# Kernel tuning notes

Hardware: AMD Instinct MI355X
Metric: run time of the kernel (lower is better)

Reference implementation:

```python
import jax, jax.numpy as jnp
import numpy as np

DT_SCALER = 1.0 / 24.0
ODE_STEPS = 4  # fixed-step RK4 stand-in for adaptive odeint(rtol=atol=1e-3)
B, T, D, H = 1024, 100, 32, 256
ODE_MID = 50  # hidden width of the ODE func MLP (hard-coded 50 in source)


def setup_inputs() -> dict:
    key = jax.random.key(0)
    ks = jax.random.split(key, 20)
    n = lambda k, s: jax.random.normal(k, s, dtype=jnp.float32)
    std = 0.1  # module inits weights N(0, 0.1), biases 0
    return {
        "dt": jax.random.uniform(ks[0], (B, T, 2), dtype=jnp.float32),
        "x": n(ks[1], (B, T, D)),
        # RNNCell params
        "W_ih": n(ks[2], (H, D)) * std,
        "b_ih": jnp.zeros((H,), jnp.float32),
        "W_hh": n(ks[3], (H, H)) * std,
        "b_hh": jnp.zeros((H,), jnp.float32),
        # ODE func: Linear(H,50) -> tanh -> Linear(50,H)
        "ode_w1": n(ks[4], (ODE_MID, H)) * std,
        "ode_b1": jnp.zeros((ODE_MID,), jnp.float32),
        "ode_w2": n(ks[5], (H, ODE_MID)) * std,
        "ode_b2": jnp.zeros((H,), jnp.float32),
        # mu head: l1 (H -> H//2), distribution_mu (H//2 -> 1)
        "l1_w": n(ks[6], (H // 2, H)) * std,
        "l1_b": jnp.zeros((H // 2,), jnp.float32),
        "mu_w": n(ks[7], (1, H // 2)) * std,
        "mu_b": jnp.zeros((1,), jnp.float32),
        # sigma head: Linear(H,H) -> tanh -> Linear(H,1) -> softplus
        "sig_w1": n(ks[8], (H, H)) * std,
        "sig_b1": jnp.zeros((H,), jnp.float32),
        "sig_w2": n(ks[9], (1, H)) * std,
        "sig_b2": jnp.zeros((1,), jnp.float32),
    }


def reference(dt, x, W_ih, b_ih, W_hh, b_hh, ode_w1, ode_b1, ode_w2, ode_b2,
              l1_w, l1_b, mu_w, mu_b, sig_w1, sig_b1, sig_w2, sig_b2):
    Bsz = x.shape[0]
    xs = jnp.swapaxes(x, 0, 1)                               # [T,B,D]
    dts = jnp.swapaxes(dt[:, :, 1] - dt[:, :, 0], 0, 1)[..., None]  # [T,B,1]
    h0 = jnp.zeros((Bsz, W_hh.shape[0]), x.dtype)
    hs = 1.0 / ODE_STEPS

    def ode_f(y, scale):
        # net(y) * (dt * DT_SCALER); RHS is time-independent
        return (jnp.tanh(y @ ode_w1.T + ode_b1) @ ode_w2.T + ode_b2) * scale

    def step(h, inp):
        x_i, dt_i = inp                                      # [B,D], [B,1]
        # h_t = h_t + RNNCell(x_i, h_t)
        h = h + jnp.tanh(x_i @ W_ih.T + b_ih + h @ W_hh.T + b_hh)
        scale = dt_i * DT_SCALER
        # integrate dh/dt = ode_f(h) from t=0 to t=1 (fixed-step RK4)
        def rk4(y, _):
            k1 = ode_f(y, scale)
            k2 = ode_f(y + 0.5 * hs * k1, scale)
            k3 = ode_f(y + 0.5 * hs * k2, scale)
            k4 = ode_f(y + hs * k3, scale)
            return y + (hs / 6.0) * (k1 + 2.0 * k2 + 2.0 * k3 + k4), None
        h, _ = jax.lax.scan(rk4, h, None, length=ODE_STEPS)
        # heads (eval mode: dropout is identity)
        mu = jax.nn.relu(h @ l1_w.T + l1_b) @ mu_w.T + mu_b              # [B,1]
        sig = jax.nn.softplus(jnp.tanh(h @ sig_w1.T + sig_b1) @ sig_w2.T + sig_b2)
        return h, (mu, sig)

    _, (mu_seq, sig_seq) = jax.lax.scan(step, h0, (xs, dts))
    mu_out = jnp.swapaxes(mu_seq, 0, 1)    # [B,T,1]
    sig_out = jnp.swapaxes(sig_seq, 0, 1)  # [B,T,1]
    return (mu_out, sig_out)
```

## Files before the change

### kernel.cpp

```cpp
#include <hip/hip_runtime.h>
#include <math.h>


#define NT 512

#define WS_WCAT 0
#define WS_L1P  73728
#define WS_SW1  106496
#define WS_TOT  172032

#define SM_PR1 0
#define SM_PR2 10240
#define SM_H   20480
#define SM_YC  21504
#define SM_AC  22528
#define SM_MD  23552
#define SM_X4  23808
#define SM_BC  23936
#define SM_OB1 24192
#define SM_OB2 24256
#define SM_L1B 24512
#define SM_SB1 24640
#define SM_MUW 24896
#define SM_SW2 25024
#define SM_SCL 25280
#define SM_TOT 25288
#define SMEM_BYTES (SM_TOT * 4)

__device__ __forceinline__ float fma4(float acc, float4 y, float4 w) {
  acc = fmaf(y.x, w.x, acc);
  acc = fmaf(y.y, w.y, acc);
  acc = fmaf(y.z, w.z, acc);
  acc = fmaf(y.w, w.w, acc);
  return acc;
}

__device__ __forceinline__ float tfast(float x) {
  float ax = fabsf(x);
  float e  = __expf(-2.f * ax);
  float t  = (1.f - e) * __builtin_amdgcn_rcpf(1.f + e);
  return copysignf(t, x);
}

__global__ void prep_transpose(const float* __restrict__ Wih,
                               const float* __restrict__ Whh,
                               const float* __restrict__ l1w,
                               const float* __restrict__ sw1,
                               float* __restrict__ ws) {
  int i = blockIdx.x * 256 + threadIdx.x;
  if (i < 73728) {
    int g = i >> 10, rem = i & 1023, j = rem >> 2, c = rem & 3;
    int k = 4 * g + c;
    ws[i] = (k < 32) ? Wih[j * 32 + k] : Whh[j * 256 + (k - 32)];
  } else if (i < 106496) {
    int t = i - 73728;
    int g = t >> 9, rem = t & 511, j = rem >> 2, c = rem & 3;
    ws[i] = l1w[j * 256 + 4 * g + c];
  } else if (i < WS_TOT) {
    int t = i - 106496;
    int g = t >> 10, rem = t & 1023, j = rem >> 2, c = rem & 3;
    ws[i] = sw1[j * 256 + 4 * g + c];
  }
}

__global__ __attribute__((amdgpu_flat_work_group_size(NT, NT)))
__attribute__((amdgpu_waves_per_eu(2)))
void odernn_main(const float* __restrict__ dt,
                 const float* __restrict__ x,
                 const float* __restrict__ bih,
                 const float* __restrict__ bhh,
                 const float* __restrict__ ow1,
                 const float* __restrict__ ob1g,
                 const float* __restrict__ ow2,
                 const float* __restrict__ ob2g,
                 const float* __restrict__ l1bg,
                 const float* __restrict__ muwg,
                 const float* __restrict__ mubg,
                 const float* __restrict__ sb1g,
                 const float* __restrict__ sw2g,
                 const float* __restrict__ sb2g,
                 const float* __restrict__ ws,
                 float* __restrict__ out) {
  extern __shared__ __align__(16) float sm[];
  const int tid = threadIdx.x;
  const int wv = tid >> 6, ln = tid & 63;
  const int b0 = blockIdx.x * 4;

  float* prS  = sm + SM_PR1;
  float* prS2 = sm + SM_PR2;
  float* hS   = sm + SM_H;
  float* ycS  = sm + SM_YC;
  float* acS  = sm + SM_AC;
  float* mdS  = sm + SM_MD;
  float* x4S  = sm + SM_X4;
  float* bcS  = sm + SM_BC;
  float* ob1S = sm + SM_OB1;
  float* ob2S = sm + SM_OB2;
  float* l1bS = sm + SM_L1B;
  float* sb1S = sm + SM_SB1;
  float* muwS = sm + SM_MUW;
  float* sw2S = sm + SM_SW2;
  float* sclS = sm + SM_SCL;
  float* l1oS = ycS;
  float* sgS  = acS;

  float4* pr1_4 = (float4*)prS;
  float4* pr2_4 = (float4*)prS2;
  const float4* h44 = (const float4*)hS;
  const float4* yc44 = (const float4*)ycS;
  const float4* md4 = (const float4*)mdS;
  const float4* x44 = (const float4*)x4S;

  const float4* wcat4 = (const float4*)(ws + WS_WCAT);
  const float4* l1w4  = (const float4*)(ws + WS_L1P);
  const float4* sw14  = (const float4*)(ws + WS_SW1);

  const int q1 = tid & 15, kc1 = tid >> 4;
  const int cq2 = tid & 63, kc2 = tid >> 6;
  float4 w1r[4][2];
  float4 w2r[4][2];
  {
#pragma unroll
    for (int n = 0; n < 4; ++n) {
      int row = 4 * q1 + n;
#pragma unroll
      for (int g = 0; g < 2; ++g) {
        if (row < 50)
          w1r[n][g] = *(const float4*)&ow1[row * 256 + kc1 * 8 + 4 * g];
        else
          w1r[n][g] = make_float4(0.f, 0.f, 0.f, 0.f);
      }
    }
    float w2tmp[4];
#pragma unroll
    for (int n = 0; n < 4; ++n) {
      int col = 4 * cq2 + n;
#pragma unroll
      for (int g = 0; g < 2; ++g) {
#pragma unroll
        for (int c = 0; c < 4; ++c) {
          int k = kc2 * 8 + 4 * g + c;
          w2tmp[c] = (k < 50) ? ow2[col * 50 + k] : 0.f;
        }
        w2r[n][g] = make_float4(w2tmp[0], w2tmp[1], w2tmp[2], w2tmp[3]);
      }
    }
  }

  if (tid < 256) {
    bcS[tid]  = bih[tid] + bhh[tid];
    ob2S[tid] = ob2g[tid];
    sb1S[tid] = sb1g[tid];
    sw2S[tid] = sw2g[tid];
  }
  if (tid < 64)  ob1S[tid] = (tid < 50) ? ob1g[tid] : 0.f;
  if (tid < 128) { l1bS[tid] = l1bg[tid]; muwS[tid] = muwg[tid]; }
  hS[tid] = 0.f; hS[tid + 512] = 0.f;
  __syncthreads();

  const float mub = mubg[0], sb2 = sb2g[0];

  for (int t = 0; t < 100; ++t) {
    if (tid < 128) {
      int r = tid >> 5, kk = tid & 31;
      x4S[r * 32 + kk] = x[((size_t)(b0 + r) * 100 + t) * 32 + kk];
    }
    if (tid < 4) {
      const float* dp = dt + ((size_t)(b0 + tid) * 100 + t) * 2;
      sclS[tid] = (dp[1] - dp[0]) * (1.f / 24.f);
    }
    __syncthreads();

    {
      const int jq = tid & 63, kc = tid >> 6;
      float4 acc0 = make_float4(0, 0, 0, 0), acc1 = acc0, acc2 = acc0, acc3 = acc0;
#pragma unroll 3
      for (int gg = 0; gg < 9; ++gg) {
        int g = kc * 9 + gg;
        float4 w0 = wcat4[g * 256 + 4 * jq + 0];
        float4 w1 = wcat4[g * 256 + 4 * jq + 1];
        float4 w2 = wcat4[g * 256 + 4 * jq + 2];
        float4 w3 = wcat4[g * 256 + 4 * jq + 3];
        float4 y0 = (g < 8) ? x44[0 * 8 + g] : h44[0 * 64 + (g - 8)];
        float4 y1 = (g < 8) ? x44[1 * 8 + g] : h44[1 * 64 + (g - 8)];
        float4 y2 = (g < 8) ? x44[2 * 8 + g] : h44[2 * 64 + (g - 8)];
        float4 y3 = (g < 8) ? x44[3 * 8 + g] : h44[3 * 64 + (g - 8)];
        acc0.x = fma4(acc0.x, y0, w0); acc0.y = fma4(acc0.y, y0, w1);
        acc0.z = fma4(acc0.z, y0, w2); acc0.w = fma4(acc0.w, y0, w3);
        acc1.x = fma4(acc1.x, y1, w0); acc1.y = fma4(acc1.y, y1, w1);
        acc1.z = fma4(acc1.z, y1, w2); acc1.w = fma4(acc1.w, y1, w3);
        acc2.x = fma4(acc2.x, y2, w0); acc2.y = fma4(acc2.y, y2, w1);
        acc2.z = fma4(acc2.z, y2, w2); acc2.w = fma4(acc2.w, y2, w3);
        acc3.x = fma4(acc3.x, y3, w0); acc3.y = fma4(acc3.y, y3, w1);
        acc3.z = fma4(acc3.z, y3, w2); acc3.w = fma4(acc3.w, y3, w3);
      }
      pr1_4[tid * 5 + 0] = acc0;
      pr1_4[tid * 5 + 1] = acc1;
      pr1_4[tid * 5 + 2] = acc2;
      pr1_4[tid * 5 + 3] = acc3;
    }
    __syncthreads();
    {
#pragma unroll
      for (int oo = 0; oo < 2; ++oo) {
        int o = tid + oo * 512;
        int r = o >> 8, j = o & 255;
        int q = j >> 2, n = j & 3;
        float s = bcS[j];
#pragma unroll
        for (int kc = 0; kc < 8; ++kc)
          s += prS[(kc * 64 + q) * 20 + r * 4 + n];
        hS[o] += tfast(s);
      }
    }
    __syncthreads();

#pragma unroll 1
    for (int os = 0; os < 4; ++os) {
#pragma unroll
      for (int s = 0; s < 4; ++s) {
        {
          const float4* ysrc = (s == 0) ? h44 : yc44;
          float4 a0 = make_float4(0, 0, 0, 0), a1 = a0, a2 = a0, a3 = a0;
#pragma unroll
          for (int g = 0; g < 2; ++g) {
            float4 y0 = ysrc[0 * 64 + kc1 * 2 + g];
            float4 y1 = ysrc[1 * 64 + kc1 * 2 + g];
            float4 y2 = ysrc[2 * 64 + kc1 * 2 + g];
            float4 y3 = ysrc[3 * 64 + kc1 * 2 + g];
            a0.x = fma4(a0.x, y0, w1r[0][g]); a0.y = fma4(a0.y, y0, w1r[1][g]);
            a0.z = fma4(a0.z, y0, w1r[2][g]); a0.w = fma4(a0.w, y0, w1r[3][g]);
            a1.x = fma4(a1.x, y1, w1r[0][g]); a1.y = fma4(a1.y, y1, w1r[1][g]);
            a1.z = fma4(a1.z, y1, w1r[2][g]); a1.w = fma4(a1.w, y1, w1r[3][g]);
            a2.x = fma4(a2.x, y2, w1r[0][g]); a2.y = fma4(a2.y, y2, w1r[1][g]);
            a2.z = fma4(a2.z, y2, w1r[2][g]); a2.w = fma4(a2.w, y2, w1r[3][g]);
            a3.x = fma4(a3.x, y3, w1r[0][g]); a3.y = fma4(a3.y, y3, w1r[1][g]);
            a3.z = fma4(a3.z, y3, w1r[2][g]); a3.w = fma4(a3.w, y3, w1r[3][g]);
          }
          pr1_4[tid * 5 + 0] = a0;
          pr1_4[tid * 5 + 1] = a1;
          pr1_4[tid * 5 + 2] = a2;
          pr1_4[tid * 5 + 3] = a3;
        }
        __syncthreads();
        if (tid < 256) {
          int r = tid >> 6, j = tid & 63;
          int q = j >> 2, n = j & 3;
          float sv = ob1S[j];
#pragma unroll
          for (int kc = 0; kc < 32; ++kc)
            sv += prS[(kc * 16 + q) * 20 + r * 4 + n];
          mdS[r * 64 + j] = tfast(sv);
        }
        __syncthreads();
        {
          float4 b0v = make_float4(0, 0, 0, 0), b1v = b0v, b2v = b0v, b3v = b0v;
#pragma unroll
          for (int g = 0; g < 2; ++g) {
            float4 m0 = md4[0 * 16 + kc2 * 2 + g];
            float4 m1 = md4[1 * 16 + kc2 * 2 + g];
            float4 m2 = md4[2 * 16 + kc2 * 2 + g];
            float4 m3 = md4[3 * 16 + kc2 * 2 + g];
            b0v.x = fma4(b0v.x, m0, w2r[0][g]); b0v.y = fma4(b0v.y, m0, w2r[1][g]);
            b0v.z = fma4(b0v.z, m0, w2r[2][g]); b0v.w = fma4(b0v.w, m0, w2r[3][g]);
            b1v.x = fma4(b1v.x, m1, w2r[0][g]); b1v.y = fma4(b1v.y, m1, w2r[1][g]);
            b1v.z = fma4(b1v.z, m1, w2r[2][g]); b1v.w = fma4(b1v.w, m1, w2r[3][g]);
            b2v.x = fma4(b2v.x, m2, w2r[0][g]); b2v.y = fma4(b2v.y, m2, w2r[1][g]);
            b2v.z = fma4(b2v.z, m2, w2r[2][g]); b2v.w = fma4(b2v.w, m2, w2r[3][g]);
            b3v.x = fma4(b3v.x, m3, w2r[0][g]); b3v.y = fma4(b3v.y, m3, w2r[1][g]);
            b3v.z = fma4(b3v.z, m3, w2r[2][g]); b3v.w = fma4(b3v.w, m3, w2r[3][g]);
          }
          pr2_4[tid * 5 + 0] = b0v;
          pr2_4[tid * 5 + 1] = b1v;
          pr2_4[tid * 5 + 2] = b2v;
          pr2_4[tid * 5 + 3] = b3v;
        }
        __syncthreads();
        {
#pragma unroll
          for (int oo = 0; oo < 2; ++oo) {
            int o = tid + oo * 512;
            int r = o >> 8, j = o & 255;
            int q = j >> 2, n = j & 3;
            float sv = ob2S[j];
#pragma unroll
            for (int kc = 0; kc < 8; ++kc)
              sv += prS2[(kc * 64 + q) * 20 + r * 4 + n];
            float kv = sv * sclS[r];
            if (s == 0)      { acS[o] = kv;        ycS[o] = hS[o] + 0.125f * kv; }
            else if (s == 1) { acS[o] += 2.f * kv; ycS[o] = hS[o] + 0.125f * kv; }
            else if (s == 2) { acS[o] += 2.f * kv; ycS[o] = hS[o] + 0.25f  * kv; }
            else             { hS[o] += (0.25f / 6.f) * (acS[o] + kv); }
          }
        }
        __syncthreads();
      }
    }

    {
      const int cq = tid & 31, kc = tid >> 5;
      float4 c0 = make_float4(0, 0, 0, 0), c1 = c0, c2 = c0, c3 = c0;
#pragma unroll 2
      for (int g = 0; g < 4; ++g) {
        int kg = kc * 4 + g;
        float4 w0 = l1w4[kg * 128 + 4 * cq + 0];
        float4 w1 = l1w4[kg * 128 + 4 * cq + 1];
        float4 w2 = l1w4[kg * 128 + 4 * cq + 2];
        float4 w3 = l1w4[kg * 128 + 4 * cq + 3];
        float4 y0 = h44[0 * 64 + kg], y1 = h44[1 * 64 + kg];
        float4 y2 = h44[2 * 64 + kg], y3 = h44[3 * 64 + kg];
        c0.x = fma4(c0.x, y0, w0); c0.y = fma4(c0.y, y0, w1);
        c0.z = fma4(c0.z, y0, w2); c0.w = fma4(c0.w, y0, w3);
        c1.x = fma4(c1.x, y1, w0); c1.y = fma4(c1.y, y1, w1);
        c1.z = fma4(c1.z, y1, w2); c1.w = fma4(c1.w, y1, w3);
        c2.x = fma4(c2.x, y2, w0); c2.y = fma4(c2.y, y2, w1);
        c2.z = fma4(c2.z, y2, w2); c2.w = fma4(c2.w, y2, w3);
        c3.x = fma4(c3.x, y3, w0); c3.y = fma4(c3.y, y3, w1);
        c3.z = fma4(c3.z, y3, w2); c3.w = fma4(c3.w, y3, w3);
      }
      pr1_4[tid * 5 + 0] = c0;
      pr1_4[tid * 5 + 1] = c1;
      pr1_4[tid * 5 + 2] = c2;
      pr1_4[tid * 5 + 3] = c3;
    }
    {
      const int cq = tid & 63, kc = tid >> 6;
      float4 d0 = make_float4(0, 0, 0, 0), d1 = d0, d2 = d0, d3 = d0;
#pragma unroll 2
      for (int g = 0; g < 8; ++g) {
        int kg = kc * 8 + g;
        float4 w0 = sw14[kg * 256 + 4 * cq + 0];
        float4 w1 = sw14[kg * 256 + 4 * cq + 1];
        float4 w2 = sw14[kg * 256 + 4 * cq + 2];
        float4 w3 = sw14[kg * 256 + 4 * cq + 3];
        float4 y0 = h44[0 * 64 + kg], y1 = h44[1 * 64 + kg];
        float4 y2 = h44[2 * 64 + kg], y3 = h44[3 * 64 + kg];
        d0.x = fma4(d0.x, y0, w0); d0.y = fma4(d0.y, y0, w1);
        d0.z = fma4(d0.z, y0, w2); d0.w = fma4(d0.w, y0, w3);
        d1.x = fma4(d1.x, y1, w0); d1.y = fma4(d1.y, y1, w1);
        d1.z = fma4(d1.z, y1, w2); d1.w = fma4(d1.w, y1, w3);
        d2.x = fma4(d2.x, y2, w0); d2.y = fma4(d2.y, y2, w1);
        d2.z = fma4(d2.z, y2, w2); d2.w = fma4(d2.w, y2, w3);
        d3.x = fma4(d3.x, y3, w0); d3.y = fma4(d3.y, y3, w1);
        d3.z = fma4(d3.z, y3, w2); d3.w = fma4(d3.w, y3, w3);
      }
      pr2_4[tid * 5 + 0] = d0;
      pr2_4[tid * 5 + 1] = d1;
      pr2_4[tid * 5 + 2] = d2;
      pr2_4[tid * 5 + 3] = d3;
    }
    __syncthreads();
    {
      int r = tid >> 7, j2 = tid & 127;
      int q = j2 >> 2, nn = j2 & 3;
      float s = l1bS[j2];
#pragma unroll
      for (int kc = 0; kc < 16; ++kc)
        s += prS[(kc * 32 + q) * 20 + r * 4 + nn];
      l1oS[r * 128 + j2] = fmaxf(s, 0.f);
    }
    {
#pragma unroll
      for (int oo = 0; oo < 2; ++oo) {
        int o = tid + oo * 512;
        int r = o >> 8, j = o & 255;
        int q = j >> 2, nn = j & 3;
        float s = sb1S[j];
#pragma unroll
        for (int kc = 0; kc < 8; ++kc)
          s += prS2[(kc * 64 + q) * 20 + r * 4 + nn];
        sgS[o] = tfast(s);
      }
    }
    __syncthreads();
    {
      const int r = wv & 3;
      if (wv < 4) {
        float pm = l1oS[r * 128 + ln] * muwS[ln]
                 + l1oS[r * 128 + 64 + ln] * muwS[64 + ln];
#pragma unroll
        for (int off = 32; off > 0; off >>= 1) pm += __shfl_down(pm, off);
        if (ln == 0) out[(size_t)(b0 + r) * 100 + t] = pm + mub;
      } else {
        float ps = sgS[r * 256 + ln] * sw2S[ln]
                 + sgS[r * 256 + 64 + ln] * sw2S[64 + ln]
                 + sgS[r * 256 + 128 + ln] * sw2S[128 + ln]
                 + sgS[r * 256 + 192 + ln] * sw2S[192 + ln];
#pragma unroll
        for (int off = 32; off > 0; off >>= 1) ps += __shfl_down(ps, off);
        if (ln == 0) {
          float z = ps + sb2;
          float sp = fmaxf(z, 0.f) + log1pf(expf(-fabsf(z)));
          out[(size_t)102400 + (size_t)(b0 + r) * 100 + t] = sp;
        }
      }
    }
  }
}

extern "C" void kernel_launch(void* const* d_in, const int* in_sizes, int n_in,
                              void* d_out, int out_size, void* d_ws, size_t ws_size,
                              hipStream_t stream) {
  const float* dt  = (const float*)d_in[0];
  const float* x   = (const float*)d_in[1];
  const float* Wih = (const float*)d_in[2];
  const float* bih = (const float*)d_in[3];
  const float* Whh = (const float*)d_in[4];
  const float* bhh = (const float*)d_in[5];
  const float* ow1 = (const float*)d_in[6];
  const float* ob1 = (const float*)d_in[7];
  const float* ow2 = (const float*)d_in[8];
  const float* ob2 = (const float*)d_in[9];
  const float* l1w = (const float*)d_in[10];
  const float* l1b = (const float*)d_in[11];
  const float* muw = (const float*)d_in[12];
  const float* mub = (const float*)d_in[13];
  const float* sw1 = (const float*)d_in[14];
  const float* sb1 = (const float*)d_in[15];
  const float* sw2 = (const float*)d_in[16];
  const float* sb2 = (const float*)d_in[17];
  float* ws  = (float*)d_ws;
  float* out = (float*)d_out;

  hipFuncSetAttribute((const void*)odernn_main,
                      hipFuncAttributeMaxDynamicSharedMemorySize, SMEM_BYTES);

  prep_transpose<<<WS_TOT / 256, 256, 0, stream>>>(Wih, Whh, l1w, sw1, ws);
  odernn_main<<<256, NT, SMEM_BYTES, stream>>>(dt, x, bih, bhh, ow1, ob1, ow2, ob2,
                                               l1b, muw, mub, sb1, sw2, sb2, ws, out);
}
```

Baseline: 3.592 ms.

## Software-pipeline RK4 stages across two row pairs and keep ODE state in registers

The RK4 loop now splits the 4 batch rows into two pairs (P and Q) and interleaves their stages, so the layer-1 partials of one pair are computed while the other pair is being reduced. This cuts barriers per RK stage from four to roughly two per pair. Per-row h and the RK accumulator now live in registers instead of shared memory, the layer-1 reduction uses DPP lane adds, and shared-memory partial buffers are padded (strides 17/33/65) to avoid bank conflicts. The next timestep's x and dt are prefetched during the tail, and the waves_per_eu hint is dropped. The cost is more complex control flow, with fewer threads active in the reduction phases.

After: 4.077 ms. 13.5% more time.

```diff
diff --git a/kernel.cpp b/kernel.cpp
--- a/kernel.cpp
+++ b/kernel.cpp
@@ -9,44 +9,73 @@
 #define WS_SW1  106496
 #define WS_TOT  172032
 
-#define SM_PR1 0
-#define SM_PR2 10240
-#define SM_H   20480
-#define SM_YC  21504
-#define SM_AC  22528
-#define SM_MD  23552
-#define SM_X4  23808
-#define SM_BC  23936
-#define SM_OB1 24192
-#define SM_OB2 24256
-#define SM_L1B 24512
-#define SM_SB1 24640
-#define SM_MUW 24896
-#define SM_SW2 25024
-#define SM_SCL 25280
-#define SM_TOT 25288
-#define SMEM_BYTES (SM_TOT * 4)
+#define F4_PR1P 0
+#define F4_PR1Q 1088
+#define F4_PR2P 2176
+#define F4_PR2Q 3216
+#define F4_PRR  2176
+#define F4_PH1  0
+#define F4_PH2  2176
+#define F4_YCP  4256
+#define F4_YCQ  4384
+#define F4_MIDP 4512
+#define F4_MIDQ 4544
+#define F4_HS   4576
+#define F4_XS   4832
+#define F4_L1O  4864
+#define F4_SG   4992
+#define F4_END  5248
+#define SM_BC   (F4_END * 4)
+#define SM_OB1  (SM_BC + 256)
+#define SM_OB2  (SM_OB1 + 64)
+#define SM_L1B  (SM_OB2 + 256)
+#define SM_SB1  (SM_L1B + 128)
+#define SM_MUW  (SM_SB1 + 256)
+#define SM_SW2  (SM_MUW + 128)
+#define SM_SCL  (SM_SW2 + 256)
+#define SM_TOTF (SM_SCL + 8)
+#define SMEM_BYTES (SM_TOTF * 4)
 
 __device__ __forceinline__ float fma4(float acc, float4 y, float4 w) {
-  acc = fmaf(y.x, w.x, acc);
-  acc = fmaf(y.y, w.y, acc);
-  acc = fmaf(y.z, w.z, acc);
-  acc = fmaf(y.w, w.w, acc);
+  acc = fmaf(y.x, w.x, acc); acc = fmaf(y.y, w.y, acc);
+  acc = fmaf(y.z, w.z, acc); acc = fmaf(y.w, w.w, acc);
   return acc;
 }
-
+__device__ __forceinline__ float4 add4(float4 a, float4 b) {
+  return make_float4(a.x + b.x, a.y + b.y, a.z + b.z, a.w + b.w);
+}
+__device__ __forceinline__ float4 axpy4(float a, float4 xv, float4 yv) {
+  return make_float4(fmaf(a, xv.x, yv.x), fmaf(a, xv.y, yv.y),
+                     fmaf(a, xv.z, yv.z), fmaf(a, xv.w, yv.w));
+}
+__device__ __forceinline__ float4 muls4(float4 v, float s) {
+  return make_float4(v.x * s, v.y * s, v.z * s, v.w * s);
+}
 __device__ __forceinline__ float tfast(float x) {
   float ax = fabsf(x);
   float e  = __expf(-2.f * ax);
   float t  = (1.f - e) * __builtin_amdgcn_rcpf(1.f + e);
   return copysignf(t, x);
 }
-
-__global__ void prep_transpose(const float* __restrict__ Wih,
-                               const float* __restrict__ Whh,
-                               const float* __restrict__ l1w,
-                               const float* __restrict__ sw1,
-                               float* __restrict__ ws) {
+__device__ __forceinline__ float4 tfast4(float4 v) {
+  return make_float4(tfast(v.x), tfast(v.y), tfast(v.z), tfast(v.w));
+}
+template <int CTRL>
+__device__ __forceinline__ float dpp_add(float v) {
+  int s = __builtin_amdgcn_update_dpp(0, __float_as_int(v), CTRL, 0xF, 0xF, true);
+  return v + __int_as_float(s);
+}
+__device__ __forceinline__ float4 red4f4(float4 v) {
+  v.x = dpp_add<0xB1>(v.x); v.y = dpp_add<0xB1>(v.y);
+  v.z = dpp_add<0xB1>(v.z); v.w = dpp_add<0xB1>(v.w);
+  v.x = dpp_add<0x4E>(v.x); v.y = dpp_add<0x4E>(v.y);
+  v.z = dpp_add<0x4E>(v.z); v.w = dpp_add<0x4E>(v.w);
+  return v;
+}
+
+__global__ void prep_w(const float* __restrict__ Wih, const float* __restrict__ Whh,
+                       const float* __restrict__ l1w, const float* __restrict__ sw1,
+                       float* __restrict__ ws) {
   int i = blockIdx.x * 256 + threadIdx.x;
   if (i < 73728) {
     int g = i >> 10, rem = i & 1023, j = rem >> 2, c = rem & 3;
@@ -64,7 +93,6 @@
 }
 
 __global__ __attribute__((amdgpu_flat_work_group_size(NT, NT)))
-__attribute__((amdgpu_waves_per_eu(2)))
 void odernn_main(const float* __restrict__ dt,
                  const float* __restrict__ x,
                  const float* __restrict__ bih,
@@ -82,38 +110,14 @@
                  const float* __restrict__ ws,
                  float* __restrict__ out) {
   extern __shared__ __align__(16) float sm[];
+  float4* f4 = (float4*)sm;
   const int tid = threadIdx.x;
-  const int wv = tid >> 6, ln = tid & 63;
   const int b0 = blockIdx.x * 4;
-
-  float* prS  = sm + SM_PR1;
-  float* prS2 = sm + SM_PR2;
-  float* hS   = sm + SM_H;
-  float* ycS  = sm + SM_YC;
-  float* acS  = sm + SM_AC;
-  float* mdS  = sm + SM_MD;
-  float* x4S  = sm + SM_X4;
-  float* bcS  = sm + SM_BC;
-  float* ob1S = sm + SM_OB1;
-  float* ob2S = sm + SM_OB2;
-  float* l1bS = sm + SM_L1B;
-  float* sb1S = sm + SM_SB1;
-  float* muwS = sm + SM_MUW;
-  float* sw2S = sm + SM_SW2;
-  float* sclS = sm + SM_SCL;
-  float* l1oS = ycS;
-  float* sgS  = acS;
-
-  float4* pr1_4 = (float4*)prS;
-  float4* pr2_4 = (float4*)prS2;
-  const float4* h44 = (const float4*)hS;
-  const float4* yc44 = (const float4*)ycS;
-  const float4* md4 = (const float4*)mdS;
-  const float4* x44 = (const float4*)x4S;
 
   const float4* wcat4 = (const float4*)(ws + WS_WCAT);
   const float4* l1w4  = (const float4*)(ws + WS_L1P);
   const float4* sw14  = (const float4*)(ws + WS_SW1);
+  const float4* xg4   = (const float4*)x;
 
   const int q1 = tid & 15, kc1 = tid >> 4;
   const int cq2 = tid & 63, kc2 = tid >> 6;
@@ -148,32 +152,104 @@
   }
 
   if (tid < 256) {
-    bcS[tid]  = bih[tid] + bhh[tid];
-    ob2S[tid] = ob2g[tid];
-    sb1S[tid] = sb1g[tid];
-    sw2S[tid] = sw2g[tid];
+    sm[SM_BC + tid]  = bih[tid] + bhh[tid];
+    sm[SM_OB2 + tid] = ob2g[tid];
+    sm[SM_SB1 + tid] = sb1g[tid];
+    sm[SM_SW2 + tid] = sw2g[tid];
   }
-  if (tid < 64)  ob1S[tid] = (tid < 50) ? ob1g[tid] : 0.f;
-  if (tid < 128) { l1bS[tid] = l1bg[tid]; muwS[tid] = muwg[tid]; }
-  hS[tid] = 0.f; hS[tid + 512] = 0.f;
+  if (tid < 64)  sm[SM_OB1 + tid] = (tid < 50) ? ob1g[tid] : 0.f;
+  if (tid < 128) { sm[SM_L1B + tid] = l1bg[tid]; sm[SM_MUW + tid] = muwg[tid]; }
+  if (tid < 256) f4[F4_HS + tid] = make_float4(0.f, 0.f, 0.f, 0.f);
+  if (tid < 32) {
+    int r = tid >> 3, g = tid & 7;
+    f4[F4_XS + tid] = xg4[((size_t)(b0 + r) * 100) * 8 + g];
+  } else if (tid < 36) {
+    int r = tid - 32;
+    const float* dp = dt + ((size_t)(b0 + r) * 100) * 2;
+    sm[SM_SCL + r] = (dp[1] - dp[0]) * (1.f / 24.f);
+  }
   __syncthreads();
 
-  const float mub = mubg[0], sb2 = sb2g[0];
+  const float mubv = mubg[0], sb2v = sb2g[0];
+  const float4* bc4   = (const float4*)(sm + SM_BC);
+  const float4* ob1_4 = (const float4*)(sm + SM_OB1);
+  const float4* ob2_4 = (const float4*)(sm + SM_OB2);
+  const float4* l1b4  = (const float4*)(sm + SM_L1B);
+  const float4* sb14  = (const float4*)(sm + SM_SB1);
+  const float4* muw4  = (const float4*)(sm + SM_MUW);
+  const float4* sw24  = (const float4*)(sm + SM_SW2);
+
+  const int cqS = tid & 63, rxS = (tid >> 6) & 1;
+  float4 hP = make_float4(0, 0, 0, 0), acP = hP, hQ = hP, acQ = hP;
+  float scP = 0.f, scQ = 0.f;
+
+  const int wv = tid >> 6, ln = tid & 63;
+
+  auto L1PART = [&](int ycB, int prB) {
+    float4 p0 = make_float4(0, 0, 0, 0), p1 = p0;
+#pragma unroll
+    for (int g = 0; g < 2; ++g) {
+      float4 y0 = f4[ycB + kc1 * 2 + g];
+      float4 y1 = f4[ycB + 64 + kc1 * 2 + g];
+      p0.x = fma4(p0.x, y0, w1r[0][g]); p0.y = fma4(p0.y, y0, w1r[1][g]);
+      p0.z = fma4(p0.z, y0, w1r[2][g]); p0.w = fma4(p0.w, y0, w1r[3][g]);
+      p1.x = fma4(p1.x, y1, w1r[0][g]); p1.y = fma4(p1.y, y1, w1r[1][g]);
+      p1.z = fma4(p1.z, y1, w1r[2][g]); p1.w = fma4(p1.w, y1, w1r[3][g]);
+    }
+    f4[prB + (kc1 * 2 + 0) * 17 + q1] = p0;
+    f4[prB + (kc1 * 2 + 1) * 17 + q1] = p1;
+  };
+  auto L1RED = [&](int prB, int midB) {
+    const int qr = (tid >> 2) & 15, sub = tid & 3, rx = tid >> 6;
+    float4 v = make_float4(0, 0, 0, 0);
+#pragma unroll
+    for (int i = 0; i < 8; ++i)
+      v = add4(v, f4[prB + ((sub * 8 + i) * 2 + rx) * 17 + qr]);
+    v = red4f4(v);
+    if (sub == 0)
+      f4[midB + rx * 16 + qr] = tfast4(add4(v, ob1_4[qr]));
+  };
+  auto L2PART = [&](int midB, int prB) {
+    float4 p0 = make_float4(0, 0, 0, 0), p1 = p0;
+#pragma unroll
+    for (int g = 0; g < 2; ++g) {
+      float4 m0 = f4[midB + kc2 * 2 + g];
+      float4 m1 = f4[midB + 16 + kc2 * 2 + g];
+      p0.x = fma4(p0.x, m0, w2r[0][g]); p0.y = fma4(p0.y, m0, w2r[1][g]);
+      p0.z = fma4(p0.z, m0, w2r[2][g]); p0.w = fma4(p0.w, m0, w2r[3][g]);
+      p1.x = fma4(p1.x, m1, w2r[0][g]); p1.y = fma4(p1.y, m1, w2r[1][g]);
+      p1.z = fma4(p1.z, m1, w2r[2][g]); p1.w = fma4(p1.w, m1, w2r[3][g]);
+    }
+    f4[prB + (kc2 * 2 + 0) * 65 + cq2] = p0;
+    f4[prB + (kc2 * 2 + 1) * 65 + cq2] = p1;
+  };
+  auto L2RED = [&](float4& h, float4& ac, float sc, int prB, int ycB,
+                   int hsRow, int e) {
+    float4 v = ob2_4[cqS];
+#pragma unroll
+    for (int i = 0; i < 8; ++i)
+      v = add4(v, f4[prB + (i * 2 + rxS) * 65 + cqS]);
+    float4 kv = muls4(v, sc);
+    const int s = e & 3;
+    float4 ycw;
+    if (s == 0) {
+      ac = kv;                      ycw = axpy4(0.125f, kv, h);
+    } else if (s == 1) {
+      ac = axpy4(2.f, kv, ac);      ycw = axpy4(0.125f, kv, h);
+    } else if (s == 2) {
+      ac = axpy4(2.f, kv, ac);      ycw = axpy4(0.25f, kv, h);
+    } else {
+      h = axpy4(0.25f / 6.f, add4(ac, kv), h);
+      ycw = h;
+    }
+    f4[ycB + rxS * 64 + cqS] = ycw;
+    if (e == 15) f4[F4_HS + hsRow * 64 + cqS] = h;
+  };
 
   for (int t = 0; t < 100; ++t) {
-    if (tid < 128) {
-      int r = tid >> 5, kk = tid & 31;
-      x4S[r * 32 + kk] = x[((size_t)(b0 + r) * 100 + t) * 32 + kk];
-    }
-    if (tid < 4) {
-      const float* dp = dt + ((size_t)(b0 + tid) * 100 + t) * 2;
-      sclS[tid] = (dp[1] - dp[0]) * (1.f / 24.f);
-    }
-    __syncthreads();
-
     {
       const int jq = tid & 63, kc = tid >> 6;
-      float4 acc0 = make_float4(0, 0, 0, 0), acc1 = acc0, acc2 = acc0, acc3 = acc0;
+      float4 a0 = make_float4(0, 0, 0, 0), a1 = a0, a2 = a0, a3 = a0;
 #pragma unroll 3
       for (int gg = 0; gg < 9; ++gg) {
         int g = kc * 9 + gg;
@@ -181,121 +257,75 @@
         float4 w1 = wcat4[g * 256 + 4 * jq + 1];
         float4 w2 = wcat4[g * 256 + 4 * jq + 2];
         float4 w3 = wcat4[g * 256 + 4 * jq + 3];
-        float4 y0 = (g < 8) ? x44[0 * 8 + g] : h44[0 * 64 + (g - 8)];
-        float4 y1 = (g < 8) ? x44[1 * 8 + g] : h44[1 * 64 + (g - 8)];
-        float4 y2 = (g < 8) ? x44[2 * 8 + g] : h44[2 * 64 + (g - 8)];
-        float4 y3 = (g < 8) ? x44[3 * 8 + g] : h44[3 * 64 + (g - 8)];
-        acc0.x = fma4(acc0.x, y0, w0); acc0.y = fma4(acc0.y, y0, w1);
-        acc0.z = fma4(acc0.z, y0, w2); acc0.w = fma4(acc0.w, y0, w3);
-        acc1.x = fma4(acc1.x, y1, w0); acc1.y = fma4(acc1.y, y1, w1);
-        acc1.z = fma4(acc1.z, y1, w2); acc1.w = fma4(acc1.w, y1, w3);
-        acc2.x = fma4(acc2.x, y2, w0); acc2.y = fma4(acc2.y, y2, w1);
-        acc2.z = fma4(acc2.z, y2, w2); acc2.w = fma4(acc2.w, y2, w3);
-        acc3.x = fma4(acc3.x, y3, w0); acc3.y = fma4(acc3.y, y3, w1);
-        acc3.z = fma4(acc3.z, y3, w2); acc3.w = fma4(acc3.w, y3, w3);
-      }
-      pr1_4[tid * 5 + 0] = acc0;
-      pr1_4[tid * 5 + 1] = acc1;
-      pr1_4[tid * 5 + 2] = acc2;
-      pr1_4[tid * 5 + 3] = acc3;
-    }
-    __syncthreads();
-    {
-#pragma unroll
-      for (int oo = 0; oo < 2; ++oo) {
-        int o = tid + oo * 512;
-        int r = o >> 8, j = o & 255;
-        int q = j >> 2, n = j & 3;
-        float s = bcS[j];
-#pragma unroll
-        for (int kc = 0; kc < 8; ++kc)
-          s += prS[(kc * 64 + q) * 20 + r * 4 + n];
-        hS[o] += tfast(s);
-      }
+        float4 y0 = (g < 8) ? f4[F4_XS + g]      : f4[F4_HS + (g - 8)];
+        float4 y1 = (g < 8) ? f4[F4_XS + 8 + g]  : f4[F4_HS + 64 + (g - 8)];
+        float4 y2 = (g < 8) ? f4[F4_XS + 16 + g] : f4[F4_HS + 128 + (g - 8)];
+        float4 y3 = (g < 8) ? f4[F4_XS + 24 + g] : f4[F4_HS + 192 + (g - 8)];
+        a0.x = fma4(a0.x, y0, w0); a0.y = fma4(a0.y, y0, w1);
+        a0.z = fma4(a0.z, y0, w2); a0.w = fma4(a0.w, y0, w3);
+        a1.x = fma4(a1.x, y1, w0); a1.y = fma4(a1.y, y1, w1);
+        a1.z = fma4(a1.z, y1, w2); a1.w = fma4(a1.w, y1, w3);
+        a2.x = fma4(a2.x, y2, w0); a2.y = fma4(a2.y, y2, w1);
+        a2.z = fma4(a2.z, y2, w2); a2.w = fma4(a2.w, y2, w3);
+        a3.x = fma4(a3.x, y3, w0); a3.y = fma4(a3.y, y3, w1);
+        a3.z = fma4(a3.z, y3, w2); a3.w = fma4(a3.w, y3, w3);
+      }
+      f4[F4_PRR + (kc * 4 + 0) * 65 + jq] = a0;
+      f4[F4_PRR + (kc * 4 + 1) * 65 + jq] = a1;
+      f4[F4_PRR + (kc * 4 + 2) * 65 + jq] = a2;
+      f4[F4_PRR + (kc * 4 + 3) * 65 + jq] = a3;
+    }
+    __syncthreads();
+    if (tid < 256) {
+      const int r = tid >> 6, jq = tid & 63;
+      float4 v = bc4[jq];
+#pragma unroll
+      for (int kc = 0; kc < 8; ++kc)
+        v = add4(v, f4[F4_PRR + (kc * 4 + r) * 65 + jq]);
+      float4 hn = add4(f4[F4_HS + r * 64 + jq], tfast4(v));
+      if (r < 2) f4[F4_YCP + r * 64 + jq] = hn;
+      else       f4[F4_YCQ + (r - 2) * 64 + jq] = hn;
     }
     __syncthreads();
 
 #pragma unroll 1
-    for (int os = 0; os < 4; ++os) {
-#pragma unroll
-      for (int s = 0; s < 4; ++s) {
-        {
-          const float4* ysrc = (s == 0) ? h44 : yc44;
-          float4 a0 = make_float4(0, 0, 0, 0), a1 = a0, a2 = a0, a3 = a0;
-#pragma unroll
-          for (int g = 0; g < 2; ++g) {
-            float4 y0 = ysrc[0 * 64 + kc1 * 2 + g];
-            float4 y1 = ysrc[1 * 64 + kc1 * 2 + g];
-            float4 y2 = ysrc[2 * 64 + kc1 * 2 + g];
-            float4 y3 = ysrc[3 * 64 + kc1 * 2 + g];
-            a0.x = fma4(a0.x, y0, w1r[0][g]); a0.y = fma4(a0.y, y0, w1r[1][g]);
-            a0.z = fma4(a0.z, y0, w1r[2][g]); a0.w = fma4(a0.w, y0, w1r[3][g]);
-            a1.x = fma4(a1.x, y1, w1r[0][g]); a1.y = fma4(a1.y, y1, w1r[1][g]);
-            a1.z = fma4(a1.z, y1, w1r[2][g]); a1.w = fma4(a1.w, y1, w1r[3][g]);
-            a2.x = fma4(a2.x, y2, w1r[0][g]); a2.y = fma4(a2.y, y2, w1r[1][g]);
-            a2.z = fma4(a2.z, y2, w1r[2][g]); a2.w = fma4(a2.w, y2, w1r[3][g]);
-            a3.x = fma4(a3.x, y3, w1r[0][g]); a3.y = fma4(a3.y, y3, w1r[1][g]);
-            a3.z = fma4(a3.z, y3, w1r[2][g]); a3.w = fma4(a3.w, y3, w1r[3][g]);
-          }
-          pr1_4[tid * 5 + 0] = a0;
-          pr1_4[tid * 5 + 1] = a1;
-          pr1_4[tid * 5 + 2] = a2;
-          pr1_4[tid * 5 + 3] = a3;
+    for (int e = 0; e < 16; ++e) {
+      L1PART(F4_YCP, F4_PR1P);
+      if (tid < 128) {
+        if (e == 0) {
+          hP = f4[F4_YCP + rxS * 64 + cqS];
+          hQ = f4[F4_YCQ + rxS * 64 + cqS];
+          acP = make_float4(0, 0, 0, 0); acQ = acP;
+          scP = sm[SM_SCL + rxS];
+          scQ = sm[SM_SCL + 2 + rxS];
+        } else {
+          L2RED(hQ, acQ, scQ, F4_PR2Q, F4_YCQ, 2 + rxS, e - 1);
         }
-        __syncthreads();
-        if (tid < 256) {
-          int r = tid >> 6, j = tid & 63;
-          int q = j >> 2, n = j & 3;
-          float sv = ob1S[j];
-#pragma unroll
-          for (int kc = 0; kc < 32; ++kc)
-            sv += prS[(kc * 16 + q) * 20 + r * 4 + n];
-          mdS[r * 64 + j] = tfast(sv);
-        }
-        __syncthreads();
-        {
-          float4 b0v = make_float4(0, 0, 0, 0), b1v = b0v, b2v = b0v, b3v = b0v;
-#pragma unroll
-          for (int g = 0; g < 2; ++g) {
-            float4 m0 = md4[0 * 16 + kc2 * 2 + g];
-            float4 m1 = md4[1 * 16 + kc2 * 2 + g];
-            float4 m2 = md4[2 * 16 + kc2 * 2 + g];
-            float4 m3 = md4[3 * 16 + kc2 * 2 + g];
-            b0v.x = fma4(b0v.x, m0, w2r[0][g]); b0v.y = fma4(b0v.y, m0, w2r[1][g]);
-            b0v.z = fma4(b0v.z, m0, w2r[2][g]); b0v.w = fma4(b0v.w, m0, w2r[3][g]);
-            b1v.x = fma4(b1v.x, m1, w2r[0][g]); b1v.y = fma4(b1v.y, m1, w2r[1][g]);
-            b1v.z = fma4(b1v.z, m1, w2r[2][g]); b1v.w = fma4(b1v.w, m1, w2r[3][g]);
-            b2v.x = fma4(b2v.x, m2, w2r[0][g]); b2v.y = fma4(b2v.y, m2, w2r[1][g]);
-            b2v.z = fma4(b2v.z, m2, w2r[2][g]); b2v.w = fma4(b2v.w, m2, w2r[3][g]);
-            b3v.x = fma4(b3v.x, m3, w2r[0][g]); b3v.y = fma4(b3v.y, m3, w2r[1][g]);
-            b3v.z = fma4(b3v.z, m3, w2r[2][g]); b3v.w = fma4(b3v.w, m3, w2r[3][g]);
-          }
-          pr2_4[tid * 5 + 0] = b0v;
-          pr2_4[tid * 5 + 1] = b1v;
-          pr2_4[tid * 5 + 2] = b2v;
-          pr2_4[tid * 5 + 3] = b3v;
-        }
-        __syncthreads();
-        {
-#pragma unroll
-          for (int oo = 0; oo < 2; ++oo) {
-            int o = tid + oo * 512;
-            int r = o >> 8, j = o & 255;
-            int q = j >> 2, n = j & 3;
-            float sv = ob2S[j];
-#pragma unroll
-            for (int kc = 0; kc < 8; ++kc)
-              sv += prS2[(kc * 64 + q) * 20 + r * 4 + n];
-            float kv = sv * sclS[r];
-            if (s == 0)      { acS[o] = kv;        ycS[o] = hS[o] + 0.125f * kv; }
-            else if (s == 1) { acS[o] += 2.f * kv; ycS[o] = hS[o] + 0.125f * kv; }
-            else if (s == 2) { acS[o] += 2.f * kv; ycS[o] = hS[o] + 0.25f  * kv; }
-            else             { hS[o] += (0.25f / 6.f) * (acS[o] + kv); }
-          }
-        }
-        __syncthreads();
-      }
-    }
+      }
+      __syncthreads();
+      L1PART(F4_YCQ, F4_PR1Q);
+      if (tid < 128) L1RED(F4_PR1P, F4_MIDP);
+      __syncthreads();
+      L2PART(F4_MIDP, F4_PR2P);
+      if (tid < 128) L1RED(F4_PR1Q, F4_MIDQ);
+      __syncthreads();
+      L2PART(F4_MIDQ, F4_PR2Q);
+      if (tid < 128) L2RED(hP, acP, scP, F4_PR2P, F4_YCP, 0 + rxS, e);
+      __syncthreads();
+    }
+    if (tid < 128) {
+      L2RED(hQ, acQ, scQ, F4_PR2Q, F4_YCQ, 2 + rxS, 15);
+    } else if (t < 99) {
+      if (tid < 160) {
+        int idx = tid - 128, r = idx >> 3, g = idx & 7;
+        f4[F4_XS + idx] = xg4[((size_t)(b0 + r) * 100 + t + 1) * 8 + g];
+      } else if (tid < 164) {
+        int r = tid - 160;
+        const float* dp = dt + ((size_t)(b0 + r) * 100 + t + 1) * 2;
+        sm[SM_SCL + r] = (dp[1] - dp[0]) * (1.f / 24.f);
+      }
+    }
+    __syncthreads();
 
     {
       const int cq = tid & 31, kc = tid >> 5;
@@ -307,8 +337,8 @@
         float4 w1 = l1w4[kg * 128 + 4 * cq + 1];
         float4 w2 = l1w4[kg * 128 + 4 * cq + 2];
         float4 w3 = l1w4[kg * 128 + 4 * cq + 3];
-        float4 y0 = h44[0 * 64 + kg], y1 = h44[1 * 64 + kg];
-        float4 y2 = h44[2 * 64 + kg], y3 = h44[3 * 64 + kg];
+        float4 y0 = f4[F4_HS + kg],       y1 = f4[F4_HS + 64 + kg];
+        float4 y2 = f4[F4_HS + 128 + kg], y3 = f4[F4_HS + 192 + kg];
         c0.x = fma4(c0.x, y0, w0); c0.y = fma4(c0.y, y0, w1);
         c0.z = fma4(c0.z, y0, w2); c0.w = fma4(c0.w, y0, w3);
         c1.x = fma4(c1.x, y1, w0); c1.y = fma4(c1.y, y1, w1);
@@ -318,10 +348,10 @@
         c3.x = fma4(c3.x, y3, w0); c3.y = fma4(c3.y, y3, w1);
         c3.z = fma4(c3.z, y3, w2); c3.w = fma4(c3.w, y3, w3);
       }
-      pr1_4[tid * 5 + 0] = c0;
-      pr1_4[tid * 5 + 1] = c1;
-      pr1_4[tid * 5 + 2] = c2;
-      pr1_4[tid * 5 + 3] = c3;
+      f4[F4_PH1 + (kc * 4 + 0) * 33 + cq] = c0;
+      f4[F4_PH1 + (kc * 4 + 1) * 33 + cq] = c1;
+      f4[F4_PH1 + (kc * 4 + 2) * 33 + cq] = c2;
+      f4[F4_PH1 + (kc * 4 + 3) * 33 + cq] = c3;
     }
     {
       const int cq = tid & 63, kc = tid >> 6;
@@ -333,8 +363,8 @@
         float4 w1 = sw14[kg * 256 + 4 * cq + 1];
         float4 w2 = sw14[kg * 256 + 4 * cq + 2];
         float4 w3 = sw14[kg * 256 + 4 * cq + 3];
-        float4 y0 = h44[0 * 64 + kg], y1 = h44[1 * 64 + kg];
-        float4 y2 = h44[2 * 64 + kg], y3 = h44[3 * 64 + kg];
+        float4 y0 = f4[F4_HS + kg],       y1 = f4[F4_HS + 64 + kg];
+        float4 y2 = f4[F4_HS + 128 + kg], y3 = f4[F4_HS + 192 + kg];
         d0.x = fma4(d0.x, y0, w0); d0.y = fma4(d0.y, y0, w1);
         d0.z = fma4(d0.z, y0, w2); d0.w = fma4(d0.w, y0, w3);
         d1.x = fma4(d1.x, y1, w0); d1.y = fma4(d1.y, y1, w1);
@@ -344,57 +374,55 @@
         d3.x = fma4(d3.x, y3, w0); d3.y = fma4(d3.y, y3, w1);
         d3.z = fma4(d3.z, y3, w2); d3.w = fma4(d3.w, y3, w3);
       }
-      pr2_4[tid * 5 + 0] = d0;
-      pr2_4[tid * 5 + 1] = d1;
-      pr2_4[tid * 5 + 2] = d2;
-      pr2_4[tid * 5 + 3] = d3;
-    }
-    __syncthreads();
-    {
-      int r = tid >> 7, j2 = tid & 127;
-      int q = j2 >> 2, nn = j2 & 3;
-      float s = l1bS[j2];
+      f4[F4_PH2 + (kc * 4 + 0) * 65 + cq] = d0;
+      f4[F4_PH2 + (kc * 4 + 1) * 65 + cq] = d1;
+      f4[F4_PH2 + (kc * 4 + 2) * 65 + cq] = d2;
+      f4[F4_PH2 + (kc * 4 + 3) * 65 + cq] = d3;
+    }
+    __syncthreads();
+    if (tid < 128) {
+      const int r = tid >> 5, cq = tid & 31;
+      float4 v = l1b4[cq];
 #pragma unroll
       for (int kc = 0; kc < 16; ++kc)
-        s += prS[(kc * 32 + q) * 20 + r * 4 + nn];
-      l1oS[r * 128 + j2] = fmaxf(s, 0.f);
-    }
-    {
-#pragma unroll
-      for (int oo = 0; oo < 2; ++oo) {
-        int o = tid + oo * 512;
-        int r = o >> 8, j = o & 255;
-        int q = j >> 2, nn = j & 3;
-        float s = sb1S[j];
-#pragma unroll
-        for (int kc = 0; kc < 8; ++kc)
-          s += prS2[(kc * 64 + q) * 20 + r * 4 + nn];
-        sgS[o] = tfast(s);
-      }
-    }
-    __syncthreads();
-    {
-      const int r = wv & 3;
-      if (wv < 4) {
-        float pm = l1oS[r * 128 + ln] * muwS[ln]
-                 + l1oS[r * 128 + 64 + ln] * muwS[64 + ln];
-#pragma unroll
-        for (int off = 32; off > 0; off >>= 1) pm += __shfl_down(pm, off);
-        if (ln == 0) out[(size_t)(b0 + r) * 100 + t] = pm + mub;
-      } else {
-        float ps = sgS[r * 256 + ln] * sw2S[ln]
-                 + sgS[r * 256 + 64 + ln] * sw2S[64 + ln]
-                 + sgS[r * 256 + 128 + ln] * sw2S[128 + ln]
-                 + sgS[r * 256 + 192 + ln] * sw2S[192 + ln];
-#pragma unroll
-        for (int off = 32; off > 0; off >>= 1) ps += __shfl_down(ps, off);
-        if (ln == 0) {
-          float z = ps + sb2;
-          float sp = fmaxf(z, 0.f) + log1pf(expf(-fabsf(z)));
-          out[(size_t)102400 + (size_t)(b0 + r) * 100 + t] = sp;
-        }
-      }
-    }
+        v = add4(v, f4[F4_PH1 + (kc * 4 + r) * 33 + cq]);
+      f4[F4_L1O + r * 32 + cq] =
+          make_float4(fmaxf(v.x, 0.f), fmaxf(v.y, 0.f),
+                      fmaxf(v.z, 0.f), fmaxf(v.w, 0.f));
+    } else if (tid < 384) {
+      const int t2 = tid - 128;
+      const int r = t2 >> 6, cq = t2 & 63;
+      float4 v = sb14[cq];
+#pragma unroll
+      for (int kc = 0; kc < 8; ++kc)
+        v = add4(v, f4[F4_PH2 + (kc * 4 + r) * 65 + cq]);
+      f4[F4_SG + r * 64 + cq] = tfast4(v);
+    }
+    __syncthreads();
+    if (wv < 4) {
+      float pm = 0.f;
+      if (ln < 32) {
+        float4 l = f4[F4_L1O + wv * 32 + ln];
+        float4 w = muw4[ln];
+        pm = l.x * w.x + l.y * w.y + l.z * w.z + l.w * w.w;
+      }
+#pragma unroll
+      for (int off = 32; off > 0; off >>= 1) pm += __shfl_down(pm, off);
+      if (ln == 0) out[(size_t)(b0 + wv) * 100 + t] = pm + mubv;
+    } else {
+      const int r = wv - 4;
+      float4 sv = f4[F4_SG + r * 64 + ln];
+      float4 w = sw24[ln];
+      float ps = sv.x * w.x + sv.y * w.y + sv.z * w.z + sv.w * w.w;
+#pragma unroll
+      for (int off = 32; off > 0; off >>= 1) ps += __shfl_down(ps, off);
+      if (ln == 0) {
+        float z = ps + sb2v;
+        float sp = fmaxf(z, 0.f) + log1pf(expf(-fabsf(z)));
+        out[(size_t)102400 + (size_t)(b0 + r) * 100 + t] = sp;
+      }
+    }
+    __syncthreads();
   }
 }
 
@@ -425,7 +453,7 @@
   hipFuncSetAttribute((const void*)odernn_main,
                       hipFuncAttributeMaxDynamicSharedMemorySize, SMEM_BYTES);
 
-  prep_transpose<<<WS_TOT / 256, 256, 0, stream>>>(Wih, Whh, l1w, sw1, ws);
+  prep_w<<<WS_TOT / 256, 256, 0, stream>>>(Wih, Whh, l1w, sw1, ws);
   odernn_main<<<256, NT, SMEM_BYTES, stream>>>(dt, x, bih, bhh, ow1, ob1, ow2, ob2,
                                                l1b, muw, mub, sb1, sw2, sb2, ws, out);
 }
```
